# Optimization experiments

Measured on AMD Instinct MI355X. Metric: run time of the kernel, lower is better.

The kernel has to match this reference:

```python
import jax, jax.numpy as jnp
import numpy as np

N, TO, TI, H = 8, 2048, 2048, 128
MASK_FILL = -99999.0  # module uses -99999.0, not -inf


def setup_inputs() -> dict:
    key = jax.random.key(0)
    kq, kv, km = jax.random.split(key, 3)
    queries = jax.random.normal(kq, (N, TO, H), dtype=jnp.float32)
    values = jax.random.normal(kv, (N, TI, H), dtype=jnp.float32)
    # mask is applied to scores.view(-1, Ti) -> shape (N*To, Ti), True = masked
    mask = jax.random.randint(km, (N * TO, TI), 0, 2).astype(bool)
    return {"queries": queries, "values": values, "mask": mask}


def reference(queries, values, mask):
    n, to, h = queries.shape
    ti = values.shape[1]
    # N x To x Ti scores (no 1/sqrt(H) scaling in the original)
    scores = jnp.einsum("nth,nsh->nts", queries, values)
    scores = jnp.where(mask.reshape(n, to, ti), MASK_FILL, scores)
    attention_distribution = jax.nn.softmax(scores, axis=-1)
    attention_output = jnp.einsum("nts,nsh->nth", attention_distribution, values)
    return attention_output, attention_distribution
```

## Files before the change

### kernel.cpp

```cpp
#include <hip/hip_runtime.h>

#define NB  8
#define TOQ 2048
#define TIV 2048
#define HD  128

typedef float f32x4 __attribute__((ext_vector_type(4)));
typedef short s16x8 __attribute__((ext_vector_type(8)));
typedef unsigned short ushort8v __attribute__((ext_vector_type(8)));

__device__ __forceinline__ unsigned short f2bf(float f) {
    unsigned u = __float_as_uint(f);
    return (unsigned short)((u + 0x7FFFu + ((u >> 16) & 1u)) >> 16);
}
__device__ __forceinline__ float bf2f(unsigned short h) {
    return __uint_as_float(((unsigned)h) << 16);
}

__device__ __forceinline__ void split8(const float4 a, const float4 b,
                                       ushort8v& h, ushort8v& l) {
    const float x[8] = {a.x, a.y, a.z, a.w, b.x, b.y, b.z, b.w};
    #pragma unroll
    for (int j = 0; j < 8; ++j) {
        const unsigned short hi = f2bf(x[j]);
        h[j] = hi;
        l[j] = f2bf(x[j] - bf2f(hi));
    }
}

__device__ __forceinline__ void gload16(const void* g, void* l) {
    __builtin_amdgcn_global_load_lds(
        (const __attribute__((address_space(1))) void*)g,
        (__attribute__((address_space(3))) void*)l, 16, 0, 0);
}

__global__ __launch_bounds__(256) void k0_split(
    const float* __restrict__ Q, const float* __restrict__ V,
    unsigned short* __restrict__ Qh, unsigned short* __restrict__ Ql,
    unsigned short* __restrict__ Vh, unsigned short* __restrict__ Vl)
{
    const size_t i = ((size_t)blockIdx.x * 256 + threadIdx.x) * 8;
    const float* src = blockIdx.y ? V : Q;
    unsigned short* dh = blockIdx.y ? Vh : Qh;
    unsigned short* dl = blockIdx.y ? Vl : Ql;
    const float4 a = *(const float4*)&src[i];
    const float4 b = *(const float4*)&src[i + 4];
    ushort8v h, l;
    split8(a, b, h, l);
    *(ushort8v*)&dh[i] = h;
    *(ushort8v*)&dl[i] = l;
}

__global__ __launch_bounds__(256) void k0_vt(
    const float* __restrict__ V, unsigned short* __restrict__ VT)
{
    __shared__ unsigned short tile[64][68];
    const int n  = blockIdx.z;
    const int s0 = blockIdx.x * 64;
    const int h0 = blockIdx.y * 64;
    const int t  = threadIdx.x;

    #pragma unroll
    for (int it = 0; it < 4; ++it) {
        const int f = t + it * 256;
        const int r = f >> 4;
        const int c = f & 15;
        const float4 v = *(const float4*)&V[((size_t)(n * TIV + s0 + r)) * HD + h0 + 4 * c];
        tile[4 * c + 0][r] = f2bf(v.x);
        tile[4 * c + 1][r] = f2bf(v.y);
        tile[4 * c + 2][r] = f2bf(v.z);
        tile[4 * c + 3][r] = f2bf(v.w);
    }
    __syncthreads();

    #pragma unroll
    for (int it = 0; it < 2; ++it) {
        const int f  = t + it * 256;
        const int hh = f >> 3;
        const int sc = f & 7;
        ushort8v o;
        #pragma unroll
        for (int j = 0; j < 8; ++j) o[j] = tile[hh][8 * sc + j];
        *(ushort8v*)&VT[((size_t)(n * HD + h0 + hh)) * TIV + s0 + 8 * sc] = o;
    }
}

__global__ __launch_bounds__(256) void k1_lds(
    const unsigned short* __restrict__ QhG, const unsigned short* __restrict__ QlG,
    const unsigned short* __restrict__ VhG, const unsigned short* __restrict__ VlG,
    const int* __restrict__ M, float* __restrict__ E,
    float* __restrict__ part)
{
    __shared__ unsigned short qh_l[128 * 32], ql_l[128 * 32];
    __shared__ unsigned short vh_l[128 * 32], vl_l[128 * 32];

    const int n    = blockIdx.z;
    const int tt   = blockIdx.y * 128;
    const int ts   = blockIdx.x * 128;
    const int t    = threadIdx.x;
    const int lane = t & 63;
    const int wave = t >> 6;
    const int wr   = wave >> 1;
    const int wc   = wave & 1;
    const int lr   = lane & 15;
    const int kg   = lane >> 4;

    f32x4 acc[4][4];
    #pragma unroll
    for (int i = 0; i < 4; ++i)
        #pragma unroll
        for (int j = 0; j < 4; ++j) acc[i][j] = (f32x4)0.f;

    for (int h0 = 0; h0 < HD; h0 += 32) {
        #pragma unroll
        for (int j = 0; j < 2; ++j) {
            const int c    = wave * 128 + j * 64 + lane;
            const int row  = c >> 2;
            const int kb   = (c & 3) * 8;
            const int lb   = (wave * 128 + j * 64) * 8;
            const size_t qo = ((size_t)(n * TOQ + tt + row)) * HD + h0 + kb;
            const size_t vo = ((size_t)(n * TIV + ts + row)) * HD + h0 + kb;
            gload16(QhG + qo, qh_l + lb);
            gload16(QlG + qo, ql_l + lb);
            gload16(VhG + vo, vh_l + lb);
            gload16(VlG + vo, vl_l + lb);
        }
        __syncthreads();

        s16x8 aH[4], aL[4];
        #pragma unroll
        for (int fm = 0; fm < 4; ++fm) {
            const int off = (wr * 64 + fm * 16 + lr) * 32 + kg * 8;
            aH[fm] = *(const s16x8*)(vh_l + off);
            aL[fm] = *(const s16x8*)(vl_l + off);
        }
        #pragma unroll
        for (int fn = 0; fn < 4; ++fn) {
            const int off = (wc * 64 + fn * 16 + lr) * 32 + kg * 8;
            const s16x8 bH = *(const s16x8*)(qh_l + off);
            const s16x8 bL = *(const s16x8*)(ql_l + off);
            #pragma unroll
            for (int fm = 0; fm < 4; ++fm) {
                acc[fm][fn] = __builtin_amdgcn_mfma_f32_16x16x32_bf16(aH[fm], bH, acc[fm][fn], 0, 0, 0);
                acc[fm][fn] = __builtin_amdgcn_mfma_f32_16x16x32_bf16(aH[fm], bL, acc[fm][fn], 0, 0, 0);
                acc[fm][fn] = __builtin_amdgcn_mfma_f32_16x16x32_bf16(aL[fm], bH, acc[fm][fn], 0, 0, 0);
            }
        }
        __syncthreads();
    }

    #pragma unroll
    for (int fn = 0; fn < 4; ++fn) {
        const int to_g = tt + wc * 64 + fn * 16 + lr;
        const size_t rowbase = ((size_t)n * TOQ + to_g) * TIV;
        float rs = 0.f;
        #pragma unroll
        for (int fm = 0; fm < 4; ++fm) {
            const int ti_g = ts + wr * 64 + fm * 16 + kg * 4;
            const int4 mv = *(const int4*)&M[rowbase + ti_g];
            float4 e;
            e.x = mv.x ? 0.f : __expf(acc[fm][fn][0]);
            e.y = mv.y ? 0.f : __expf(acc[fm][fn][1]);
            e.z = mv.z ? 0.f : __expf(acc[fm][fn][2]);
            e.w = mv.w ? 0.f : __expf(acc[fm][fn][3]);
            *(float4*)&E[rowbase + ti_g] = e;
            rs += (e.x + e.y) + (e.z + e.w);
        }
        rs += __shfl_xor(rs, 16, 64);
        rs += __shfl_xor(rs, 32, 64);
        if (kg == 0)
            part[((size_t)n * TOQ + to_g) * 32 + blockIdx.x * 2 + wr] = rs;
    }
}

__global__ __launch_bounds__(256) void k1_reg(
    const float* __restrict__ Q, const float* __restrict__ V,
    const int* __restrict__ M, float* __restrict__ E,
    float* __restrict__ part)
{
    __shared__ unsigned short qhi[128 * 32], qlo[128 * 32];
    __shared__ unsigned short vhi[128 * 32], vlo[128 * 32];

    const int n    = blockIdx.z;
    const int tt   = blockIdx.y * 128;
    const int ts   = blockIdx.x * 128;
    const int t    = threadIdx.x;
    const int lane = t & 63;
    const int wave = t >> 6;
    const int wr   = wave >> 1;
    const int wc   = wave & 1;
    const int lr   = lane & 15;
    const int kg   = lane >> 4;

    const float* Qb = Q + ((size_t)n * TOQ + tt) * HD;
    const float* Vb = V + ((size_t)n * TIV + ts) * HD;

    f32x4 acc[4][4];
    #pragma unroll
    for (int i = 0; i < 4; ++i)
        #pragma unroll
        for (int j = 0; j < 4; ++j) acc[i][j] = (f32x4)0.f;

    for (int h0 = 0; h0 < HD; h0 += 32) {
        #pragma unroll
        for (int it = 0; it < 2; ++it) {
            const int i   = t + it * 256;
            const int row = i >> 2;
            const int kb  = i & 3;
            const float* qs = Qb + (size_t)row * HD + h0 + kb * 8;
            const float* vs = Vb + (size_t)row * HD + h0 + kb * 8;
            const float4 q0 = *(const float4*)qs, q1 = *(const float4*)(qs + 4);
            const float4 v0 = *(const float4*)vs, v1 = *(const float4*)(vs + 4);
            ushort8v qh, ql, vh, vl;
            split8(q0, q1, qh, ql);
            split8(v0, v1, vh, vl);
            *(ushort8v*)(qhi + i * 8) = qh;
            *(ushort8v*)(qlo + i * 8) = ql;
            *(ushort8v*)(vhi + i * 8) = vh;
            *(ushort8v*)(vlo + i * 8) = vl;
        }
        __syncthreads();

        s16x8 aH[4], aL[4];
        #pragma unroll
        for (int fm = 0; fm < 4; ++fm) {
            const int off = (wr * 64 + fm * 16 + lr) * 32 + kg * 8;
            aH[fm] = *(const s16x8*)(vhi + off);
            aL[fm] = *(const s16x8*)(vlo + off);
        }
        #pragma unroll
        for (int fn = 0; fn < 4; ++fn) {
            const int off = (wc * 64 + fn * 16 + lr) * 32 + kg * 8;
            const s16x8 bH = *(const s16x8*)(qhi + off);
            const s16x8 bL = *(const s16x8*)(qlo + off);
            #pragma unroll
            for (int fm = 0; fm < 4; ++fm) {
                acc[fm][fn] = __builtin_amdgcn_mfma_f32_16x16x32_bf16(aH[fm], bH, acc[fm][fn], 0, 0, 0);
                acc[fm][fn] = __builtin_amdgcn_mfma_f32_16x16x32_bf16(aH[fm], bL, acc[fm][fn], 0, 0, 0);
                acc[fm][fn] = __builtin_amdgcn_mfma_f32_16x16x32_bf16(aL[fm], bH, acc[fm][fn], 0, 0, 0);
            }
        }
        __syncthreads();
    }

    #pragma unroll
    for (int fn = 0; fn < 4; ++fn) {
        const int to_g = tt + wc * 64 + fn * 16 + lr;
        const size_t rowbase = ((size_t)n * TOQ + to_g) * TIV;
        float rs = 0.f;
        #pragma unroll
        for (int fm = 0; fm < 4; ++fm) {
            const int ti_g = ts + wr * 64 + fm * 16 + kg * 4;
            const int4 mv = *(const int4*)&M[rowbase + ti_g];
            float4 e;
            e.x = mv.x ? 0.f : __expf(acc[fm][fn][0]);
            e.y = mv.y ? 0.f : __expf(acc[fm][fn][1]);
            e.z = mv.z ? 0.f : __expf(acc[fm][fn][2]);
            e.w = mv.w ? 0.f : __expf(acc[fm][fn][3]);
            *(float4*)&E[rowbase + ti_g] = e;
            rs += (e.x + e.y) + (e.z + e.w);
        }
        rs += __shfl_xor(rs, 16, 64);
        rs += __shfl_xor(rs, 32, 64);
        if (kg == 0)
            part[((size_t)n * TOQ + to_g) * 32 + blockIdx.x * 2 + wr] = rs;
    }
}

__global__ __launch_bounds__(256) void k2_rowsum(
    const float* __restrict__ part, float* __restrict__ rec)
{
    const int row = blockIdx.x * 256 + threadIdx.x;
    const float4* p4 = (const float4*)(part + (size_t)row * 32);
    float s = 0.f;
    #pragma unroll
    for (int i = 0; i < 8; ++i) {
        const float4 v = p4[i];
        s += (v.x + v.y) + (v.z + v.w);
    }
    rec[row] = 1.f / s;
}

__global__ __launch_bounds__(512) void k3_pv(
    float* __restrict__ EP, const unsigned short* __restrict__ VT,
    const float* __restrict__ rec, float* __restrict__ O)
{
    __shared__ float red[2][3][16][132];

    const int n    = blockIdx.y;
    const int r0   = blockIdx.x * 32;
    const int t    = threadIdx.x;
    const int wave = t >> 6;
    const int lane = t & 63;
    const int p    = wave >> 2;
    const int q    = wave & 3;
    const int lr   = lane & 15;
    const int kg   = lane >> 4;

    const int rowg = r0 + p * 16 + lr;
    const float rc = rec[n * TOQ + rowg];
    float* Erow = EP + ((size_t)n * TOQ + rowg) * TIV;
    const unsigned short* VTb = VT + (size_t)n * HD * TIV;

    f32x4 acc[8];
    #pragma unroll
    for (int fn = 0; fn < 8; ++fn) acc[fn] = (f32x4)0.f;

    const int kbase = q * 512 + kg * 8;

    #pragma unroll 2
    for (int k0 = 0; k0 < 512; k0 += 32) {
        const int k = kbase + k0;
        const float4 e0 = *(const float4*)&Erow[k];
        const float4 e1 = *(const float4*)&Erow[k + 4];
        float4 p0, p1;
        p0.x = e0.x * rc; p0.y = e0.y * rc; p0.z = e0.z * rc; p0.w = e0.w * rc;
        p1.x = e1.x * rc; p1.y = e1.y * rc; p1.z = e1.z * rc; p1.w = e1.w * rc;
        *(float4*)&Erow[k]     = p0;
        *(float4*)&Erow[k + 4] = p1;

        s16x8 a;
        a[0] = (short)f2bf(p0.x); a[1] = (short)f2bf(p0.y);
        a[2] = (short)f2bf(p0.z); a[3] = (short)f2bf(p0.w);
        a[4] = (short)f2bf(p1.x); a[5] = (short)f2bf(p1.y);
        a[6] = (short)f2bf(p1.z); a[7] = (short)f2bf(p1.w);

        #pragma unroll
        for (int fn = 0; fn < 8; ++fn) {
            const s16x8 b = *(const s16x8*)&VTb[(size_t)(fn * 16 + lr) * TIV + k];
            acc[fn] = __builtin_amdgcn_mfma_f32_16x16x32_bf16(a, b, acc[fn], 0, 0, 0);
        }
    }

    if (q != 0) {
        #pragma unroll
        for (int fn = 0; fn < 8; ++fn)
            #pragma unroll
            for (int ri = 0; ri < 4; ++ri)
                red[p][q - 1][kg * 4 + ri][fn * 16 + lr] = acc[fn][ri];
    }
    __syncthreads();
    if (q == 0) {
        #pragma unroll
        for (int fn = 0; fn < 8; ++fn) {
            #pragma unroll
            for (int ri = 0; ri < 4; ++ri) {
                const int orow = r0 + p * 16 + kg * 4 + ri;
                float o = acc[fn][ri];
                o += red[p][0][kg * 4 + ri][fn * 16 + lr];
                o += red[p][1][kg * 4 + ri][fn * 16 + lr];
                o += red[p][2][kg * 4 + ri][fn * 16 + lr];
                O[((size_t)n * TOQ + orow) * HD + fn * 16 + lr] = o;
            }
        }
    }
}

extern "C" void kernel_launch(void* const* d_in, const int* in_sizes, int n_in,
                              void* d_out, int out_size, void* d_ws, size_t ws_size,
                              hipStream_t stream)
{
    const float* Q = (const float*)d_in[0];
    const float* V = (const float*)d_in[1];
    const int*   M = (const int*)d_in[2];

    float* O = (float*)d_out;
    float* E = O + (size_t)NB * TOQ * HD;

    char* ws = (char*)d_ws;
    float*          recb = (float*)ws;
    float*          part = (float*)(ws + (1 << 16));
    unsigned short* VT   = (unsigned short*)(ws + (1 << 16) + (NB * TOQ * 32 * 4));

    const size_t elems   = (size_t)NB * TOQ * HD;
    const size_t sbytes  = elems * 2;
    const size_t base    = (1 << 16) + (size_t)(NB * TOQ * 32 * 4) + sbytes;
    const size_t ws_need = base + 4 * sbytes;

    k0_vt<<<dim3(TIV / 64, HD / 64, NB), 256, 0, stream>>>(V, VT);

    if (ws_size >= ws_need) {
        unsigned short* Qh = (unsigned short*)(ws + base);
        unsigned short* Ql = (unsigned short*)(ws + base + sbytes);
        unsigned short* Vh = (unsigned short*)(ws + base + 2 * sbytes);
        unsigned short* Vl = (unsigned short*)(ws + base + 3 * sbytes);
        k0_split<<<dim3((unsigned)(elems / 8 / 256), 2), 256, 0, stream>>>(Q, V, Qh, Ql, Vh, Vl);
        k1_lds  <<<dim3(TIV / 128, TOQ / 128, NB), 256, 0, stream>>>(Qh, Ql, Vh, Vl, M, E, part);
    } else {
        k1_reg  <<<dim3(TIV / 128, TOQ / 128, NB), 256, 0, stream>>>(Q, V, M, E, part);
    }

    k2_rowsum<<<dim3(NB * TOQ / 256), 256, 0, stream>>>(part, recb);
    k3_pv    <<<dim3(TOQ / 32, NB), 512, 0, stream>>>(E, VT, recb, O);
}
```

Baseline: 185.8 us.

## Pre-swizzle V^T into MFMA fragment order and stage P tiles through LDS

The V transpose kernel now writes V^T in a fragment-major layout, so each lane's B operand for the 16x16x32 MFMA is one contiguous 16-byte load and a wave reads a fully coalesced 1 KB block. In the PV kernel, each row-wise pass over E now reads contiguous 128-column chunks per lane group, writes the normalized probabilities back, and stages them as bf16 in per-wave LDS before reading A fragments. The goal is to cut strided global loads of V^T and the uncoalesced row-strided E reads. In exchange it adds LDS traffic and an extra barrier, with the staging and reduction buffers sharing the same shared memory.

```diff
diff --git a/kernel.cpp b/kernel.cpp
--- a/kernel.cpp
+++ b/kernel.cpp
@@ -52,7 +52,7 @@
 }
 
 __global__ __launch_bounds__(256) void k0_vt(
-    const float* __restrict__ V, unsigned short* __restrict__ VT)
+    const float* __restrict__ V, unsigned short* __restrict__ VTf)
 {
     __shared__ unsigned short tile[64][68];
     const int n  = blockIdx.z;
@@ -75,13 +75,18 @@
 
     #pragma unroll
     for (int it = 0; it < 2; ++it) {
-        const int f  = t + it * 256;
-        const int hh = f >> 3;
-        const int sc = f & 7;
+        const int s    = t * 2 + it;
+        const int k32i = s >> 8;
+        const int fni  = (s >> 6) & 3;
+        const int l    = s & 63;
+        const int hh   = fni * 16 + (l & 15);
+        const int kloc = k32i * 32 + ((l >> 4) * 8);
         ushort8v o;
         #pragma unroll
-        for (int j = 0; j < 8; ++j) o[j] = tile[hh][8 * sc + j];
-        *(ushort8v*)&VT[((size_t)(n * HD + h0 + hh)) * TIV + s0 + 8 * sc] = o;
+        for (int j = 0; j < 8; ++j) o[j] = tile[hh][kloc + j];
+        const size_t k32g = (size_t)(s0 >> 5) + k32i;
+        const size_t fng  = (size_t)(h0 >> 4) + fni;
+        *(ushort8v*)&VTf[(((size_t)n * 64 + k32g) * 8 + fng) * 512 + (size_t)l * 8] = o;
     }
 }
 
@@ -282,10 +287,12 @@
 }
 
 __global__ __launch_bounds__(512) void k3_pv(
-    float* __restrict__ EP, const unsigned short* __restrict__ VT,
+    float* __restrict__ EP, const unsigned short* __restrict__ VTf,
     const float* __restrict__ rec, float* __restrict__ O)
 {
-    __shared__ float red[2][3][16][132];
+    __shared__ __attribute__((aligned(16))) char smem[50688];
+    unsigned short* stg = (unsigned short*)smem;
+    float*          red = (float*)smem;
 
     const int n    = blockIdx.y;
     const int r0   = blockIdx.x * 32;
@@ -297,47 +304,60 @@
     const int lr   = lane & 15;
     const int kg   = lane >> 4;
 
-    const int rowg = r0 + p * 16 + lr;
-    const float rc = rec[n * TOQ + rowg];
-    float* Erow = EP + ((size_t)n * TOQ + rowg) * TIV;
-    const unsigned short* VTb = VT + (size_t)n * HD * TIV;
+    const size_t rowbase0 = (size_t)n * TOQ + r0 + p * 16;
+    unsigned short* wstg = stg + wave * (16 * 136);
+
+    float rv[4];
+    #pragma unroll
+    for (int r = 0; r < 4; ++r) rv[r] = rec[rowbase0 + 4 * r + kg];
 
     f32x4 acc[8];
     #pragma unroll
     for (int fn = 0; fn < 8; ++fn) acc[fn] = (f32x4)0.f;
 
-    const int kbase = q * 512 + kg * 8;
-
-    #pragma unroll 2
-    for (int k0 = 0; k0 < 512; k0 += 32) {
-        const int k = kbase + k0;
-        const float4 e0 = *(const float4*)&Erow[k];
-        const float4 e1 = *(const float4*)&Erow[k + 4];
-        float4 p0, p1;
-        p0.x = e0.x * rc; p0.y = e0.y * rc; p0.z = e0.z * rc; p0.w = e0.w * rc;
-        p1.x = e1.x * rc; p1.y = e1.y * rc; p1.z = e1.z * rc; p1.w = e1.w * rc;
-        *(float4*)&Erow[k]     = p0;
-        *(float4*)&Erow[k + 4] = p1;
-
-        s16x8 a;
-        a[0] = (short)f2bf(p0.x); a[1] = (short)f2bf(p0.y);
-        a[2] = (short)f2bf(p0.z); a[3] = (short)f2bf(p0.w);
-        a[4] = (short)f2bf(p1.x); a[5] = (short)f2bf(p1.y);
-        a[6] = (short)f2bf(p1.z); a[7] = (short)f2bf(p1.w);
-
-        #pragma unroll
-        for (int fn = 0; fn < 8; ++fn) {
-            const s16x8 b = *(const s16x8*)&VTb[(size_t)(fn * 16 + lr) * TIV + k];
-            acc[fn] = __builtin_amdgcn_mfma_f32_16x16x32_bf16(a, b, acc[fn], 0, 0, 0);
-        }
-    }
-
+    const unsigned short* VTn = VTf + (size_t)n * 64 * 8 * 512;
+
+    for (int kb = 0; kb < 4; ++kb) {
+        const int kwin = q * 512 + kb * 128;
+
+        #pragma unroll
+        for (int r = 0; r < 4; ++r) {
+            const int row_l = 4 * r + kg;
+            float* Erow = EP + (rowbase0 + row_l) * TIV + kwin + lr * 8;
+            const float4 e0 = *(const float4*)Erow;
+            const float4 e1 = *(const float4*)(Erow + 4);
+            const float rc = rv[r];
+            float4 p0, p1;
+            p0.x = e0.x * rc; p0.y = e0.y * rc; p0.z = e0.z * rc; p0.w = e0.w * rc;
+            p1.x = e1.x * rc; p1.y = e1.y * rc; p1.z = e1.z * rc; p1.w = e1.w * rc;
+            *(float4*)Erow       = p0;
+            *(float4*)(Erow + 4) = p1;
+            ushort8v s8;
+            s8[0] = f2bf(p0.x); s8[1] = f2bf(p0.y); s8[2] = f2bf(p0.z); s8[3] = f2bf(p0.w);
+            s8[4] = f2bf(p1.x); s8[5] = f2bf(p1.y); s8[6] = f2bf(p1.z); s8[7] = f2bf(p1.w);
+            *(ushort8v*)&wstg[row_l * 136 + lr * 8] = s8;
+        }
+
+        #pragma unroll
+        for (int ks = 0; ks < 4; ++ks) {
+            const s16x8 a = *(const s16x8*)&wstg[lr * 136 + ks * 32 + kg * 8];
+            const int k32 = q * 16 + kb * 4 + ks;
+            const unsigned short* bbase = VTn + ((size_t)k32 * 8) * 512 + (size_t)lane * 8;
+            #pragma unroll
+            for (int fn = 0; fn < 8; ++fn) {
+                const s16x8 b = *(const s16x8*)(bbase + (size_t)fn * 512);
+                acc[fn] = __builtin_amdgcn_mfma_f32_16x16x32_bf16(a, b, acc[fn], 0, 0, 0);
+            }
+        }
+    }
+
+    __syncthreads();
     if (q != 0) {
         #pragma unroll
         for (int fn = 0; fn < 8; ++fn)
             #pragma unroll
             for (int ri = 0; ri < 4; ++ri)
-                red[p][q - 1][kg * 4 + ri][fn * 16 + lr] = acc[fn][ri];
+                red[(((size_t)p * 3 + (q - 1)) * 16 + kg * 4 + ri) * 132 + fn * 16 + lr] = acc[fn][ri];
     }
     __syncthreads();
     if (q == 0) {
@@ -347,9 +367,9 @@
             for (int ri = 0; ri < 4; ++ri) {
                 const int orow = r0 + p * 16 + kg * 4 + ri;
                 float o = acc[fn][ri];
-                o += red[p][0][kg * 4 + ri][fn * 16 + lr];
-                o += red[p][1][kg * 4 + ri][fn * 16 + lr];
-                o += red[p][2][kg * 4 + ri][fn * 16 + lr];
+                o += red[(((size_t)p * 3 + 0) * 16 + kg * 4 + ri) * 132 + fn * 16 + lr];
+                o += red[(((size_t)p * 3 + 1) * 16 + kg * 4 + ri) * 132 + fn * 16 + lr];
+                o += red[(((size_t)p * 3 + 2) * 16 + kg * 4 + ri) * 132 + fn * 16 + lr];
                 O[((size_t)n * TOQ + orow) * HD + fn * 16 + lr] = o;
             }
         }
@@ -365,31 +385,33 @@
     const int*   M = (const int*)d_in[2];
 
     float* O = (float*)d_out;
-    float* E = O + (size_t)NB * TOQ * HD;
+    float* P = O + (size_t)NB * TOQ * HD;
 
     char* ws = (char*)d_ws;
+    const size_t partB  = (size_t)NB * TOQ * 32 * 4;
+    const size_t vtB    = (size_t)NB * 64 * 8 * 512 * 2;
+    const size_t elems  = (size_t)NB * TOQ * HD;
+    const size_t sbytes = elems * 2;
+
     float*          recb = (float*)ws;
     float*          part = (float*)(ws + (1 << 16));
-    unsigned short* VT   = (unsigned short*)(ws + (1 << 16) + (NB * TOQ * 32 * 4));
-
-    const size_t elems   = (size_t)NB * TOQ * HD;
-    const size_t sbytes  = elems * 2;
-    const size_t base    = (1 << 16) + (size_t)(NB * TOQ * 32 * 4) + sbytes;
-    const size_t ws_need = base + 4 * sbytes;
-
-    k0_vt<<<dim3(TIV / 64, HD / 64, NB), 256, 0, stream>>>(V, VT);
-
-    if (ws_size >= ws_need) {
-        unsigned short* Qh = (unsigned short*)(ws + base);
-        unsigned short* Ql = (unsigned short*)(ws + base + sbytes);
-        unsigned short* Vh = (unsigned short*)(ws + base + 2 * sbytes);
-        unsigned short* Vl = (unsigned short*)(ws + base + 3 * sbytes);
+    unsigned short* VTf  = (unsigned short*)(ws + (1 << 16) + partB);
+    const size_t splitOff = (1 << 16) + partB + vtB;
+    const size_t need1    = splitOff + 4 * sbytes;
+
+    k0_vt<<<dim3(TIV / 64, HD / 64, NB), 256, 0, stream>>>(V, VTf);
+
+    if (ws_size >= need1) {
+        unsigned short* Qh = (unsigned short*)(ws + splitOff);
+        unsigned short* Ql = (unsigned short*)(ws + splitOff + sbytes);
+        unsigned short* Vh = (unsigned short*)(ws + splitOff + 2 * sbytes);
+        unsigned short* Vl = (unsigned short*)(ws + splitOff + 3 * sbytes);
         k0_split<<<dim3((unsigned)(elems / 8 / 256), 2), 256, 0, stream>>>(Q, V, Qh, Ql, Vh, Vl);
-        k1_lds  <<<dim3(TIV / 128, TOQ / 128, NB), 256, 0, stream>>>(Qh, Ql, Vh, Vl, M, E, part);
+        k1_lds  <<<dim3(TIV / 128, TOQ / 128, NB), 256, 0, stream>>>(Qh, Ql, Vh, Vl, M, P, part);
     } else {
-        k1_reg  <<<dim3(TIV / 128, TOQ / 128, NB), 256, 0, stream>>>(Q, V, M, E, part);
+        k1_reg  <<<dim3(TIV / 128, TOQ / 128, NB), 256, 0, stream>>>(Q, V, M, P, part);
     }
 
     k2_rowsum<<<dim3(NB * TOQ / 256), 256, 0, stream>>>(part, recb);
-    k3_pv    <<<dim3(TOQ / 32, NB), 512, 0, stream>>>(E, VT, recb, O);
-}
+    k3_pv    <<<dim3(TOQ / 32, NB), 512, 0, stream>>>(P, VTf, recb, O);
+}
```

Measured after the change: 183.0 us. No clear change (-1.5%).
